# Optimization experiments

Measured on AMD Instinct MI355X. Metric: run time of the kernel, lower is better.

The kernel has to match this reference:

```python
import jax, jax.numpy as jnp
import numpy as np

SIGMA = 0.001
EPS_LOG = 1e-12
EPS_COS = 1e-8


def setup_inputs() -> dict:
    key = jax.random.key(0)
    k1, k2, k3, k4 = jax.random.split(key, 4)
    B, T, K, S, d = 32, 512, 8, 8, 300
    center_pos = jax.random.randint(k1, (B,), 0, T)
    query_token_ids = jax.random.randint(k2, (B, T), 0, 30000)
    center_sense_embeddings = jax.random.normal(k3, (B, K, d), dtype=jnp.float32)
    context_sense_embeddings = jax.random.normal(k4, (B, T - 1, S, d), dtype=jnp.float32)
    return {
        'center_pos': center_pos,
        'query_token_ids': query_token_ids,
        'center_sense_embeddings': center_sense_embeddings,
        'context_sense_embeddings': context_sense_embeddings,
    }


def reference(center_pos, query_token_ids, center_sense_embeddings, context_sense_embeddings):
    B, T = query_token_ids.shape
    d = center_sense_embeddings.shape[-1]
    # v: mean over senses of context tokens -> [B, C, d], C = T-1
    v = context_sense_embeddings.mean(axis=-2)
    # a: scaled dot between center senses and context vectors -> [B, C, K]
    a = jnp.einsum('bkd,bcd->bck', center_sense_embeddings, v) / jnp.sqrt(jnp.float32(d))
    # context positions: skip the center position (vectorized form of the per-batch loop)
    i = jnp.arange(T - 1)  # [C]
    ctx_pos = i[None, :] + (i[None, :] >= center_pos[:, None])  # [B, C]
    w = jnp.exp(-jnp.abs(ctx_pos - center_pos[:, None]).astype(jnp.float32) / SIGMA)
    logw = jnp.log(jnp.maximum(w, EPS_LOG))  # [B, C]
    alpha = jax.nn.softmax(a + logw[:, :, None], axis=1)  # softmax over context positions
    m = jnp.einsum('bck,bcd->bkd', alpha, v)  # [B, K, d]
    # cosine similarity along d (torch semantics: clamp each norm by eps)
    num = jnp.sum(center_sense_embeddings * m, axis=-1)
    n1 = jnp.linalg.norm(center_sense_embeddings, axis=-1)
    n2 = jnp.linalg.norm(m, axis=-1)
    s = num / (jnp.maximum(n1, EPS_COS) * jnp.maximum(n2, EPS_COS))  # [B, K]
    q = jax.nn.softmax(s, axis=-1)
    idx = jnp.argmax(q, axis=-1)  # [B]
    pooled = jnp.take_along_axis(center_sense_embeddings, idx[:, None, None], axis=1)[:, 0, :]  # [B, d]
    return pooled, q
```

## Files before the change

kernel.cpp:

```cpp
#include <hip/hip_runtime.h>

#define NB 32
#define NC 511
#define NK 8
#define NS 8
#define ND 300
#define ND4 75
#define NCH 8
#define CCHUNK 64
#define EPS_COS 1e-8f

__global__ __launch_bounds__(256) void k_va(const float* __restrict__ ctx,
                                            const float* __restrict__ cen,
                                            float* __restrict__ v,
                                            float* __restrict__ a) {
    int b    = blockIdx.x >> 7;
    int cgrp = blockIdx.x & 127;
    int w    = threadIdx.x >> 6;
    int lane = threadIdx.x & 63;
    int c = cgrp * 4 + w;
    if (c >= NC) return;

    const float4* ctx4 = (const float4*)ctx + (size_t)(b * NC + c) * NS * ND4;
    int i0 = lane;
    int i1 = lane + 64;
    bool has1 = (i1 < ND4);

    float4 s0 = make_float4(0.f, 0.f, 0.f, 0.f);
    float4 s1 = make_float4(0.f, 0.f, 0.f, 0.f);
#pragma unroll
    for (int s = 0; s < NS; ++s) {
        float4 x = ctx4[s * ND4 + i0];
        s0.x += x.x; s0.y += x.y; s0.z += x.z; s0.w += x.w;
        if (has1) {
            float4 y = ctx4[s * ND4 + i1];
            s1.x += y.x; s1.y += y.y; s1.z += y.z; s1.w += y.w;
        }
    }
    const float inv = 0.125f;
    s0.x *= inv; s0.y *= inv; s0.z *= inv; s0.w *= inv;
    s1.x *= inv; s1.y *= inv; s1.z *= inv; s1.w *= inv;

    float4* v4 = (float4*)v + (size_t)(b * NC + c) * ND4;
    v4[i0] = s0;
    if (has1) v4[i1] = s1;

    const float4* cen4 = (const float4*)cen + (size_t)b * NK * ND4;
    float pk[NK];
#pragma unroll
    for (int k = 0; k < NK; ++k) {
        float4 ca = cen4[k * ND4 + i0];
        float p = ca.x * s0.x + ca.y * s0.y + ca.z * s0.z + ca.w * s0.w;
        if (has1) {
            float4 cb = cen4[k * ND4 + i1];
            p += cb.x * s1.x + cb.y * s1.y + cb.z * s1.z + cb.w * s1.w;
        }
        pk[k] = p;
    }
#pragma unroll
    for (int off = 32; off; off >>= 1) {
#pragma unroll
        for (int k = 0; k < NK; ++k) pk[k] += __shfl_down(pk[k], off);
    }
    if (lane == 0) {
        const float scale = 0.057735026919f;
#pragma unroll
        for (int k = 0; k < NK; ++k)
            a[(size_t)(b * NK + k) * NC + c] = pk[k] * scale;
    }
}

__global__ __launch_bounds__(256) void k_softmax(float* __restrict__ a) {
    float* p = a + (size_t)blockIdx.x * NC;
    int t = threadIdx.x;
    int lane = t & 63, w = t >> 6;
    __shared__ float rmax[4];
    __shared__ float rsum[4];

    float x0 = (t < NC) ? p[t] : -INFINITY;
    float x1 = (t + 256 < NC) ? p[t + 256] : -INFINITY;
    float mx = fmaxf(x0, x1);
#pragma unroll
    for (int off = 32; off; off >>= 1) mx = fmaxf(mx, __shfl_xor(mx, off));
    if (lane == 0) rmax[w] = mx;
    __syncthreads();
    mx = fmaxf(fmaxf(rmax[0], rmax[1]), fmaxf(rmax[2], rmax[3]));

    float e0 = (t < NC) ? __expf(x0 - mx) : 0.f;
    float e1 = (t + 256 < NC) ? __expf(x1 - mx) : 0.f;
    float s = e0 + e1;
#pragma unroll
    for (int off = 32; off; off >>= 1) s += __shfl_xor(s, off);
    if (lane == 0) rsum[w] = s;
    __syncthreads();
    float tot = rsum[0] + rsum[1] + rsum[2] + rsum[3];
    float invt = 1.f / tot;
    if (t < NC) p[t] = e0 * invt;
    if (t + 256 < NC) p[t + 256] = e1 * invt;
}

__global__ __launch_bounds__(320) void k_m(const float* __restrict__ v,
                                           const float* __restrict__ alpha,
                                           float* __restrict__ part) {
    int b  = blockIdx.x >> 3;
    int ch = blockIdx.x & 7;
    int c0 = ch * CCHUNK;
    int cn = min(CCHUNK, NC - c0);
    __shared__ float al[NK][CCHUNK];
    int t = threadIdx.x;
    for (int idx = t; idx < NK * CCHUNK; idx += 320) {
        int k = idx / CCHUNK, cc = idx % CCHUNK;
        al[k][cc] = (cc < cn) ? alpha[(size_t)(b * NK + k) * NC + c0 + cc] : 0.f;
    }
    __syncthreads();
    if (t < ND) {
        float acc[NK] = {0.f, 0.f, 0.f, 0.f, 0.f, 0.f, 0.f, 0.f};
        const float* vp = v + ((size_t)b * NC + c0) * ND + t;
        for (int cc = 0; cc < cn; ++cc) {
            float vv = vp[(size_t)cc * ND];
#pragma unroll
            for (int k = 0; k < NK; ++k) acc[k] += al[k][cc] * vv;
        }
        float* pp = part + ((size_t)(ch * NB + b) * NK) * ND + t;
#pragma unroll
        for (int k = 0; k < NK; ++k) pp[(size_t)k * ND] = acc[k];
    }
}

__global__ __launch_bounds__(256) void k_final(const float* __restrict__ part,
                                               const float* __restrict__ cen,
                                               float* __restrict__ out) {
    int b = blockIdx.x;
    __shared__ float m[NK * ND];
    __shared__ float sred[NK];
    __shared__ int bidx;
    int t = threadIdx.x;

    for (int idx = t; idx < NK * ND; idx += 256) {
        float s = 0.f;
#pragma unroll
        for (int ch = 0; ch < NCH; ++ch)
            s += part[(size_t)(ch * NB + b) * NK * ND + idx];
        m[idx] = s;
    }
    __syncthreads();

    int w = t >> 6, lane = t & 63;
#pragma unroll
    for (int kk = 0; kk < 2; ++kk) {
        int k = w + kk * 4;
        const float* cp = cen + (size_t)(b * NK + k) * ND;
        const float* mp = m + k * ND;
        float num = 0.f, n1 = 0.f, n2 = 0.f;
        for (int dd = lane; dd < ND; dd += 64) {
            float cv = cp[dd], mv = mp[dd];
            num += cv * mv; n1 += cv * cv; n2 += mv * mv;
        }
#pragma unroll
        for (int off = 32; off; off >>= 1) {
            num += __shfl_down(num, off);
            n1  += __shfl_down(n1, off);
            n2  += __shfl_down(n2, off);
        }
        if (lane == 0) {
            float denom = fmaxf(sqrtf(n1), EPS_COS) * fmaxf(sqrtf(n2), EPS_COS);
            sred[k] = num / denom;
        }
    }
    __syncthreads();

    if (t == 0) {
        float mx = sred[0];
#pragma unroll
        for (int k = 1; k < NK; ++k) mx = fmaxf(mx, sred[k]);
        float e[NK], sum = 0.f;
#pragma unroll
        for (int k = 0; k < NK; ++k) { e[k] = __expf(sred[k] - mx); sum += e[k]; }
        float inv = 1.f / sum;
        int best = 0; float bv = sred[0];
#pragma unroll
        for (int k = 1; k < NK; ++k) if (sred[k] > bv) { bv = sred[k]; best = k; }
#pragma unroll
        for (int k = 0; k < NK; ++k)
            out[(size_t)NB * ND + b * NK + k] = e[k] * inv;
        bidx = best;
    }
    __syncthreads();

    const float* src = cen + (size_t)(b * NK + bidx) * ND;
    for (int idx = t; idx < ND; idx += 256)
        out[(size_t)b * ND + idx] = src[idx];
}

extern "C" void kernel_launch(void* const* d_in, const int* in_sizes, int n_in,
                              void* d_out, int out_size, void* d_ws, size_t ws_size,
                              hipStream_t stream) {
    const float* cen = (const float*)d_in[2];
    const float* ctx = (const float*)d_in[3];
    float* out = (float*)d_out;

    float* v    = (float*)d_ws;
    float* a    = v + (size_t)NB * NC * ND;
    float* part = a + (size_t)NB * NK * NC;

    k_va<<<dim3(NB * 128), dim3(256), 0, stream>>>(ctx, cen, v, a);
    k_softmax<<<dim3(NB * NK), dim3(256), 0, stream>>>(a);
    k_m<<<dim3(NB * NCH), dim3(320), 0, stream>>>(v, a, part);
    k_final<<<dim3(NB), dim3(256), 0, stream>>>(part, cen, out);
}
```

Baseline: 266.4 us.

## Fuse all four stages into one cooperative kernel with grid-wide syncs

Replaces the four separate launches (mean/score, softmax, weighted sum, final cosine/argmax) with one cooperative kernel of 256 blocks × 512 threads, separated by grid.sync. The goal is to remove inter-kernel launch gaps and tail effects. The final cosine stage now spreads each (b,k) pair across a whole block instead of one wave. In exchange, the first stage runs at much lower occupancy (8 waves per CU, each looping serially over 8 contexts), which may cut memory-level parallelism on the dominant context read. Each grid sync also adds its own cost.

```diff
diff --git a/kernel.cpp b/kernel.cpp
--- a/kernel.cpp
+++ b/kernel.cpp
@@ -1,4 +1,7 @@
 #include <hip/hip_runtime.h>
+#include <hip/hip_cooperative_groups.h>
+
+namespace cg = cooperative_groups;
 
 #define NB 32
 #define NC 511
@@ -10,151 +13,146 @@
 #define CCHUNK 64
 #define EPS_COS 1e-8f
 
-__global__ __launch_bounds__(256) void k_va(const float* __restrict__ ctx,
-                                            const float* __restrict__ cen,
-                                            float* __restrict__ v,
-                                            float* __restrict__ a) {
-    int b    = blockIdx.x >> 7;
-    int cgrp = blockIdx.x & 127;
-    int w    = threadIdx.x >> 6;
-    int lane = threadIdx.x & 63;
-    int c = cgrp * 4 + w;
-    if (c >= NC) return;
-
-    const float4* ctx4 = (const float4*)ctx + (size_t)(b * NC + c) * NS * ND4;
-    int i0 = lane;
-    int i1 = lane + 64;
-    bool has1 = (i1 < ND4);
-
-    float4 s0 = make_float4(0.f, 0.f, 0.f, 0.f);
-    float4 s1 = make_float4(0.f, 0.f, 0.f, 0.f);
-#pragma unroll
-    for (int s = 0; s < NS; ++s) {
-        float4 x = ctx4[s * ND4 + i0];
-        s0.x += x.x; s0.y += x.y; s0.z += x.z; s0.w += x.w;
-        if (has1) {
-            float4 y = ctx4[s * ND4 + i1];
-            s1.x += y.x; s1.y += y.y; s1.z += y.z; s1.w += y.w;
-        }
-    }
-    const float inv = 0.125f;
-    s0.x *= inv; s0.y *= inv; s0.z *= inv; s0.w *= inv;
-    s1.x *= inv; s1.y *= inv; s1.z *= inv; s1.w *= inv;
-
-    float4* v4 = (float4*)v + (size_t)(b * NC + c) * ND4;
-    v4[i0] = s0;
-    if (has1) v4[i1] = s1;
-
-    const float4* cen4 = (const float4*)cen + (size_t)b * NK * ND4;
-    float pk[NK];
-#pragma unroll
-    for (int k = 0; k < NK; ++k) {
-        float4 ca = cen4[k * ND4 + i0];
-        float p = ca.x * s0.x + ca.y * s0.y + ca.z * s0.z + ca.w * s0.w;
-        if (has1) {
-            float4 cb = cen4[k * ND4 + i1];
-            p += cb.x * s1.x + cb.y * s1.y + cb.z * s1.z + cb.w * s1.w;
-        }
-        pk[k] = p;
-    }
-#pragma unroll
-    for (int off = 32; off; off >>= 1) {
-#pragma unroll
-        for (int k = 0; k < NK; ++k) pk[k] += __shfl_down(pk[k], off);
-    }
-    if (lane == 0) {
-        const float scale = 0.057735026919f;
-#pragma unroll
-        for (int k = 0; k < NK; ++k)
-            a[(size_t)(b * NK + k) * NC + c] = pk[k] * scale;
-    }
-}
-
-__global__ __launch_bounds__(256) void k_softmax(float* __restrict__ a) {
-    float* p = a + (size_t)blockIdx.x * NC;
-    int t = threadIdx.x;
-    int lane = t & 63, w = t >> 6;
-    __shared__ float rmax[4];
-    __shared__ float rsum[4];
-
-    float x0 = (t < NC) ? p[t] : -INFINITY;
-    float x1 = (t + 256 < NC) ? p[t + 256] : -INFINITY;
-    float mx = fmaxf(x0, x1);
-#pragma unroll
-    for (int off = 32; off; off >>= 1) mx = fmaxf(mx, __shfl_xor(mx, off));
-    if (lane == 0) rmax[w] = mx;
-    __syncthreads();
-    mx = fmaxf(fmaxf(rmax[0], rmax[1]), fmaxf(rmax[2], rmax[3]));
-
-    float e0 = (t < NC) ? __expf(x0 - mx) : 0.f;
-    float e1 = (t + 256 < NC) ? __expf(x1 - mx) : 0.f;
-    float s = e0 + e1;
-#pragma unroll
-    for (int off = 32; off; off >>= 1) s += __shfl_xor(s, off);
-    if (lane == 0) rsum[w] = s;
-    __syncthreads();
-    float tot = rsum[0] + rsum[1] + rsum[2] + rsum[3];
-    float invt = 1.f / tot;
-    if (t < NC) p[t] = e0 * invt;
-    if (t + 256 < NC) p[t + 256] = e1 * invt;
-}
-
-__global__ __launch_bounds__(320) void k_m(const float* __restrict__ v,
-                                           const float* __restrict__ alpha,
-                                           float* __restrict__ part) {
-    int b  = blockIdx.x >> 3;
-    int ch = blockIdx.x & 7;
-    int c0 = ch * CCHUNK;
-    int cn = min(CCHUNK, NC - c0);
-    __shared__ float al[NK][CCHUNK];
-    int t = threadIdx.x;
-    for (int idx = t; idx < NK * CCHUNK; idx += 320) {
-        int k = idx / CCHUNK, cc = idx % CCHUNK;
-        al[k][cc] = (cc < cn) ? alpha[(size_t)(b * NK + k) * NC + c0 + cc] : 0.f;
-    }
-    __syncthreads();
-    if (t < ND) {
-        float acc[NK] = {0.f, 0.f, 0.f, 0.f, 0.f, 0.f, 0.f, 0.f};
-        const float* vp = v + ((size_t)b * NC + c0) * ND + t;
-        for (int cc = 0; cc < cn; ++cc) {
-            float vv = vp[(size_t)cc * ND];
-#pragma unroll
-            for (int k = 0; k < NK; ++k) acc[k] += al[k][cc] * vv;
-        }
-        float* pp = part + ((size_t)(ch * NB + b) * NK) * ND + t;
-#pragma unroll
-        for (int k = 0; k < NK; ++k) pp[(size_t)k * ND] = acc[k];
-    }
-}
-
-__global__ __launch_bounds__(256) void k_final(const float* __restrict__ part,
-                                               const float* __restrict__ cen,
-                                               float* __restrict__ out) {
-    int b = blockIdx.x;
-    __shared__ float m[NK * ND];
-    __shared__ float sred[NK];
-    __shared__ int bidx;
-    int t = threadIdx.x;
-
-    for (int idx = t; idx < NK * ND; idx += 256) {
-        float s = 0.f;
-#pragma unroll
-        for (int ch = 0; ch < NCH; ++ch)
-            s += part[(size_t)(ch * NB + b) * NK * ND + idx];
-        m[idx] = s;
-    }
-    __syncthreads();
-
-    int w = t >> 6, lane = t & 63;
-#pragma unroll
-    for (int kk = 0; kk < 2; ++kk) {
-        int k = w + kk * 4;
-        const float* cp = cen + (size_t)(b * NK + k) * ND;
-        const float* mp = m + k * ND;
+__global__ __launch_bounds__(512, 1) void fused(const float* __restrict__ ctx,
+                                                const float* __restrict__ cen,
+                                                float* __restrict__ v,
+                                                float* __restrict__ a,
+                                                float* __restrict__ part,
+                                                float* __restrict__ s,
+                                                float* __restrict__ out) {
+    cg::grid_group grid = cg::this_grid();
+    const int t = threadIdx.x;
+    const int lane = t & 63;
+    const int w = t >> 6;
+    const int blk = blockIdx.x;
+
+    __shared__ float sh_al[NK][CCHUNK];
+    __shared__ float sh_red[8];
+    __shared__ float sh_red3[8][3];
+    __shared__ int   sh_idx;
+
+    {
+        const int b = blk >> 3;
+        const int cbase = (blk & 7) * 64 + w * 8;
+        const float4* cen4 = (const float4*)cen + (size_t)b * NK * ND4;
+        const int i0 = lane;
+        const int i1 = lane + 64;
+        const bool has1 = (i1 < ND4);
+
+#pragma unroll 1
+        for (int u = 0; u < 8; ++u) {
+            const int c = cbase + u;
+            if (c >= NC) continue;
+
+            const float4* ctx4 = (const float4*)ctx + (size_t)(b * NC + c) * NS * ND4;
+            float4 s0 = make_float4(0.f, 0.f, 0.f, 0.f);
+            float4 s1 = make_float4(0.f, 0.f, 0.f, 0.f);
+#pragma unroll
+            for (int sj = 0; sj < NS; ++sj) {
+                float4 x = ctx4[sj * ND4 + i0];
+                s0.x += x.x; s0.y += x.y; s0.z += x.z; s0.w += x.w;
+                if (has1) {
+                    float4 y = ctx4[sj * ND4 + i1];
+                    s1.x += y.x; s1.y += y.y; s1.z += y.z; s1.w += y.w;
+                }
+            }
+            const float inv = 0.125f;
+            s0.x *= inv; s0.y *= inv; s0.z *= inv; s0.w *= inv;
+            s1.x *= inv; s1.y *= inv; s1.z *= inv; s1.w *= inv;
+
+            float4* v4 = (float4*)v + (size_t)(b * NC + c) * ND4;
+            v4[i0] = s0;
+            if (has1) v4[i1] = s1;
+
+            float pk[NK];
+#pragma unroll
+            for (int k = 0; k < NK; ++k) {
+                float4 ca = cen4[k * ND4 + i0];
+                float p = ca.x * s0.x + ca.y * s0.y + ca.z * s0.z + ca.w * s0.w;
+                if (has1) {
+                    float4 cb = cen4[k * ND4 + i1];
+                    p += cb.x * s1.x + cb.y * s1.y + cb.z * s1.z + cb.w * s1.w;
+                }
+                pk[k] = p;
+            }
+#pragma unroll
+            for (int off = 32; off; off >>= 1) {
+#pragma unroll
+                for (int k = 0; k < NK; ++k) pk[k] += __shfl_down(pk[k], off);
+            }
+            if (lane == 0) {
+                const float scale = 0.057735026919f;
+#pragma unroll
+                for (int k = 0; k < NK; ++k)
+                    a[(size_t)(b * NK + k) * NC + c] = pk[k] * scale;
+            }
+        }
+    }
+    grid.sync();
+
+    {
+        float* p = a + (size_t)blk * NC;
+        float x = (t < NC) ? p[t] : -INFINITY;
+        float mx = x;
+#pragma unroll
+        for (int off = 32; off; off >>= 1) mx = fmaxf(mx, __shfl_xor(mx, off));
+        if (lane == 0) sh_red[w] = mx;
+        __syncthreads();
+        mx = sh_red[0];
+#pragma unroll
+        for (int i = 1; i < 8; ++i) mx = fmaxf(mx, sh_red[i]);
+
+        float e = (t < NC) ? __expf(x - mx) : 0.f;
+        float ss = e;
+#pragma unroll
+        for (int off = 32; off; off >>= 1) ss += __shfl_xor(ss, off);
+        __syncthreads();
+        if (lane == 0) sh_red[w] = ss;
+        __syncthreads();
+        float tot = sh_red[0];
+#pragma unroll
+        for (int i = 1; i < 8; ++i) tot += sh_red[i];
+        if (t < NC) p[t] = e * (1.f / tot);
+    }
+    grid.sync();
+
+    {
+        const int b = blk >> 3;
+        const int ch = blk & 7;
+        const int c0 = ch * CCHUNK;
+        const int cn = min(CCHUNK, NC - c0);
+        {
+            const int k = t >> 6;
+            const int cc = t & 63;
+            sh_al[k][cc] = (cc < cn) ? a[(size_t)(b * NK + k) * NC + c0 + cc] : 0.f;
+        }
+        __syncthreads();
+        if (t < ND) {
+            float acc[NK] = {0.f, 0.f, 0.f, 0.f, 0.f, 0.f, 0.f, 0.f};
+            const float* vp = v + ((size_t)b * NC + c0) * ND + t;
+            for (int cc = 0; cc < cn; ++cc) {
+                float vv = vp[(size_t)cc * ND];
+#pragma unroll
+                for (int k = 0; k < NK; ++k) acc[k] += sh_al[k][cc] * vv;
+            }
+            float* pp = part + ((size_t)(ch * NB + b) * NK) * ND + t;
+#pragma unroll
+            for (int k = 0; k < NK; ++k) pp[(size_t)k * ND] = acc[k];
+        }
+    }
+    grid.sync();
+
+    {
+        const int b = blk >> 3;
+        const int k = blk & 7;
         float num = 0.f, n1 = 0.f, n2 = 0.f;
-        for (int dd = lane; dd < ND; dd += 64) {
-            float cv = cp[dd], mv = mp[dd];
-            num += cv * mv; n1 += cv * cv; n2 += mv * mv;
+        if (t < ND) {
+            float m = 0.f;
+#pragma unroll
+            for (int ch = 0; ch < NCH; ++ch)
+                m += part[((size_t)(ch * NB + b) * NK + k) * ND + t];
+            float cv = cen[(size_t)(b * NK + k) * ND + t];
+            num = cv * m; n1 = cv * cv; n2 = m * m;
         }
 #pragma unroll
         for (int off = 32; off; off >>= 1) {
@@ -162,34 +160,44 @@
             n1  += __shfl_down(n1, off);
             n2  += __shfl_down(n2, off);
         }
-        if (lane == 0) {
-            float denom = fmaxf(sqrtf(n1), EPS_COS) * fmaxf(sqrtf(n2), EPS_COS);
-            sred[k] = num / denom;
-        }
-    }
-    __syncthreads();
-
-    if (t == 0) {
-        float mx = sred[0];
-#pragma unroll
-        for (int k = 1; k < NK; ++k) mx = fmaxf(mx, sred[k]);
-        float e[NK], sum = 0.f;
-#pragma unroll
-        for (int k = 0; k < NK; ++k) { e[k] = __expf(sred[k] - mx); sum += e[k]; }
-        float inv = 1.f / sum;
-        int best = 0; float bv = sred[0];
-#pragma unroll
-        for (int k = 1; k < NK; ++k) if (sred[k] > bv) { bv = sred[k]; best = k; }
-#pragma unroll
-        for (int k = 0; k < NK; ++k)
-            out[(size_t)NB * ND + b * NK + k] = e[k] * inv;
-        bidx = best;
-    }
-    __syncthreads();
-
-    const float* src = cen + (size_t)(b * NK + bidx) * ND;
-    for (int idx = t; idx < ND; idx += 256)
-        out[(size_t)b * ND + idx] = src[idx];
+        if (lane == 0) { sh_red3[w][0] = num; sh_red3[w][1] = n1; sh_red3[w][2] = n2; }
+        __syncthreads();
+        if (t == 0) {
+            float a0 = 0.f, a1 = 0.f, a2 = 0.f;
+#pragma unroll
+            for (int i = 0; i < 8; ++i) { a0 += sh_red3[i][0]; a1 += sh_red3[i][1]; a2 += sh_red3[i][2]; }
+            float denom = fmaxf(sqrtf(a1), EPS_COS) * fmaxf(sqrtf(a2), EPS_COS);
+            s[b * NK + k] = a0 / denom;
+        }
+    }
+    grid.sync();
+
+    if (blk < NB) {
+        const int b = blk;
+        if (t == 0) {
+            float sv[NK];
+#pragma unroll
+            for (int k = 0; k < NK; ++k) sv[k] = s[b * NK + k];
+            float mx = sv[0];
+#pragma unroll
+            for (int k = 1; k < NK; ++k) mx = fmaxf(mx, sv[k]);
+            float e[NK], sum = 0.f;
+#pragma unroll
+            for (int k = 0; k < NK; ++k) { e[k] = __expf(sv[k] - mx); sum += e[k]; }
+            float invs = 1.f / sum;
+            int best = 0; float bv = sv[0];
+#pragma unroll
+            for (int k = 1; k < NK; ++k) if (sv[k] > bv) { bv = sv[k]; best = k; }
+#pragma unroll
+            for (int k = 0; k < NK; ++k)
+                out[(size_t)NB * ND + b * NK + k] = e[k] * invs;
+            sh_idx = best;
+        }
+        __syncthreads();
+        const float* src = cen + (size_t)(b * NK + sh_idx) * ND;
+        for (int idx = t; idx < ND; idx += 512)
+            out[(size_t)b * ND + idx] = src[idx];
+    }
 }
 
 extern "C" void kernel_launch(void* const* d_in, const int* in_sizes, int n_in,
@@ -202,9 +210,9 @@
     float* v    = (float*)d_ws;
     float* a    = v + (size_t)NB * NC * ND;
     float* part = a + (size_t)NB * NK * NC;
-
-    k_va<<<dim3(NB * 128), dim3(256), 0, stream>>>(ctx, cen, v, a);
-    k_softmax<<<dim3(NB * NK), dim3(256), 0, stream>>>(a);
-    k_m<<<dim3(NB * NCH), dim3(320), 0, stream>>>(v, a, part);
-    k_final<<<dim3(NB), dim3(256), 0, stream>>>(part, cen, out);
+    float* s    = part + (size_t)NCH * NB * NK * ND;
+
+    void* args[] = { (void*)&ctx, (void*)&cen, (void*)&v, (void*)&a,
+                     (void*)&part, (void*)&s, (void*)&out };
+    hipLaunchCooperativeKernel((void*)fused, dim3(256), dim3(512), args, 0, stream);
 }
```

Measured after the change: 400.5 us. +50.3%, slower.

## Drop softmax kernel using scale-invariance of cosine similarity; split context finer

Applied to the files above, without the earlier changes.

The attention scores are now written as plain exponentials in k_va, and the separate softmax kernel is removed. This works because the cosine similarity in k_final does not change when m is scaled, so the per-row normalisation is not needed. The context is also split into 16 chunks of 32 instead of 8 of 64 in k_m, which gives more blocks and shorter serial loops, at the cost of more partial sums for k_final to read. Skipping max subtraction could overflow for large scores, though the test's input scales keep them small.

```diff
diff --git a/kernel.cpp b/kernel.cpp
--- a/kernel.cpp
+++ b/kernel.cpp
@@ -6,14 +6,15 @@
 #define NS 8
 #define ND 300
 #define ND4 75
-#define NCH 8
-#define CCHUNK 64
+#define NCH 16
+#define CCHUNK 32
 #define EPS_COS 1e-8f
+
 
 __global__ __launch_bounds__(256) void k_va(const float* __restrict__ ctx,
                                             const float* __restrict__ cen,
                                             float* __restrict__ v,
-                                            float* __restrict__ a) {
+                                            float* __restrict__ ea) {
     int b    = blockIdx.x >> 7;
     int cgrp = blockIdx.x & 127;
     int w    = threadIdx.x >> 6;
@@ -66,51 +67,22 @@
         const float scale = 0.057735026919f;
 #pragma unroll
         for (int k = 0; k < NK; ++k)
-            a[(size_t)(b * NK + k) * NC + c] = pk[k] * scale;
+            ea[(size_t)(b * NK + k) * NC + c] = __expf(pk[k] * scale);
     }
 }
 
-__global__ __launch_bounds__(256) void k_softmax(float* __restrict__ a) {
-    float* p = a + (size_t)blockIdx.x * NC;
-    int t = threadIdx.x;
-    int lane = t & 63, w = t >> 6;
-    __shared__ float rmax[4];
-    __shared__ float rsum[4];
-
-    float x0 = (t < NC) ? p[t] : -INFINITY;
-    float x1 = (t + 256 < NC) ? p[t + 256] : -INFINITY;
-    float mx = fmaxf(x0, x1);
-#pragma unroll
-    for (int off = 32; off; off >>= 1) mx = fmaxf(mx, __shfl_xor(mx, off));
-    if (lane == 0) rmax[w] = mx;
-    __syncthreads();
-    mx = fmaxf(fmaxf(rmax[0], rmax[1]), fmaxf(rmax[2], rmax[3]));
-
-    float e0 = (t < NC) ? __expf(x0 - mx) : 0.f;
-    float e1 = (t + 256 < NC) ? __expf(x1 - mx) : 0.f;
-    float s = e0 + e1;
-#pragma unroll
-    for (int off = 32; off; off >>= 1) s += __shfl_xor(s, off);
-    if (lane == 0) rsum[w] = s;
-    __syncthreads();
-    float tot = rsum[0] + rsum[1] + rsum[2] + rsum[3];
-    float invt = 1.f / tot;
-    if (t < NC) p[t] = e0 * invt;
-    if (t + 256 < NC) p[t + 256] = e1 * invt;
-}
-
 __global__ __launch_bounds__(320) void k_m(const float* __restrict__ v,
-                                           const float* __restrict__ alpha,
+                                           const float* __restrict__ ea,
                                            float* __restrict__ part) {
-    int b  = blockIdx.x >> 3;
-    int ch = blockIdx.x & 7;
+    int b  = blockIdx.x >> 4;
+    int ch = blockIdx.x & 15;
     int c0 = ch * CCHUNK;
     int cn = min(CCHUNK, NC - c0);
     __shared__ float al[NK][CCHUNK];
     int t = threadIdx.x;
-    for (int idx = t; idx < NK * CCHUNK; idx += 320) {
-        int k = idx / CCHUNK, cc = idx % CCHUNK;
-        al[k][cc] = (cc < cn) ? alpha[(size_t)(b * NK + k) * NC + c0 + cc] : 0.f;
+    if (t < NK * CCHUNK) {
+        int k = t >> 5, cc = t & 31;
+        al[k][cc] = (cc < cn) ? ea[(size_t)(b * NK + k) * NC + c0 + cc] : 0.f;
     }
     __syncthreads();
     if (t < ND) {
@@ -200,11 +172,10 @@
     float* out = (float*)d_out;
 
     float* v    = (float*)d_ws;
-    float* a    = v + (size_t)NB * NC * ND;
-    float* part = a + (size_t)NB * NK * NC;
+    float* ea   = v + (size_t)NB * NC * ND;
+    float* part = ea + (size_t)NB * NK * NC;
 
-    k_va<<<dim3(NB * 128), dim3(256), 0, stream>>>(ctx, cen, v, a);
-    k_softmax<<<dim3(NB * NK), dim3(256), 0, stream>>>(a);
-    k_m<<<dim3(NB * NCH), dim3(320), 0, stream>>>(v, a, part);
+    k_va<<<dim3(NB * 128), dim3(256), 0, stream>>>(ctx, cen, v, ea);
+    k_m<<<dim3(NB * NCH), dim3(320), 0, stream>>>(v, ea, part);
     k_final<<<dim3(NB), dim3(256), 0, stream>>>(part, cen, out);
 }
```

Measured after the change: 256.1 us. 1.04x faster.
